# Kernel optimization log

Measured on AMD Instinct MI355X. Metric: run time of the kernel, lower is better.

The kernel has to match this reference:

```python
import jax, jax.numpy as jnp
import numpy as np

B, C, N, INPUT_DIM = 16, 19, 64, 200
VQ_DIM = 64
NUM_EMBED = 8192
FREQ = INPUT_DIM // 2 + 1  # 101 rfft bins


def setup_inputs() -> dict:
    key = jax.random.key(0)
    k_x, k_pa, k_pp, k_ca, k_cp = jax.random.split(key, 5)
    x = jax.random.normal(k_x, (B, C, N, INPUT_DIM), dtype=jnp.float32)
    # xavier_normal for [FREQ, VQ_DIM]
    std = float(np.sqrt(2.0 / (FREQ + VQ_DIM)))
    proj_amp = jax.random.normal(k_pa, (FREQ, VQ_DIM), dtype=jnp.float32) * std
    proj_phase = jax.random.normal(k_pp, (FREQ, VQ_DIM), dtype=jnp.float32) * std
    codebook_amp = jax.random.uniform(k_ca, (NUM_EMBED, VQ_DIM), dtype=jnp.float32)
    codebook_phase = jax.random.uniform(k_cp, (NUM_EMBED, VQ_DIM), dtype=jnp.float32)
    return {"x": x, "proj_amp": proj_amp, "proj_phase": proj_phase,
            "codebook_amp": codebook_amp, "codebook_phase": codebook_phase}


def _l2norm(v):
    return v / jnp.linalg.norm(v, axis=-1, keepdims=True)


def reference(x, proj_amp, proj_phase, codebook_amp, codebook_phase):
    # rfft over last dim with ortho norm -> [B,C,N,FREQ] complex
    x_fft = jnp.fft.rfft(x, axis=-1, norm="ortho")
    amp = jnp.abs(x_fft)
    phase = jnp.angle(x_fft)
    # project to vq space and L2-normalize features and codebooks
    feat_amp = _l2norm(amp @ proj_amp)        # [B,C,N,D]
    feat_phase = _l2norm(phase @ proj_phase)  # [B,C,N,D]
    cb_amp = _l2norm(codebook_amp)            # [M,D]
    cb_phase = _l2norm(codebook_phase)        # [M,D]
    # cosine similarity vs codebook, argmax over codebook axis
    sim_amp = jnp.einsum("bcnd,md->bcnm", feat_amp, cb_amp)
    sim_phase = jnp.einsum("bcnd,md->bcnm", feat_phase, cb_phase)
    idx_amp = jnp.argmax(sim_amp, axis=-1)
    idx_phase = jnp.argmax(sim_phase, axis=-1)
    return idx_amp, idx_phase
```

## Files before the change

### kernel.cpp

```cpp
#include <hip/hip_runtime.h>
#include <math.h>

constexpr int ROWS  = 19456;
constexpr int IN_DIM = 200;
constexpr int FREQ  = 101;
constexpr int VQD   = 64;
constexpr int NEMB  = 8192;
constexpr int DFT_BLOCKS = ROWS / 8;

typedef __attribute__((ext_vector_type(8))) short short8;
typedef __attribute__((ext_vector_type(4))) float floatx4;

__device__ __forceinline__ unsigned short f2bf(float v) {
    unsigned int u = __builtin_bit_cast(unsigned int, v);
    unsigned int r = u + 0x7fffu + ((u >> 16) & 1u);
    return (unsigned short)(r >> 16);
}
__device__ __forceinline__ float bf2f(unsigned short b) {
    unsigned int u = ((unsigned int)b) << 16;
    return __builtin_bit_cast(float, u);
}

__device__ __forceinline__ void cis_exact(int r, double& c, double& s) {
    if (r == 0)        { c =  1.0; s =  0.0; }
    else if (r == 50)  { c =  0.0; s = -1.0; }
    else if (r == 100) { c = -1.0; s =  0.0; }
    else if (r == 150) { c =  0.0; s =  1.0; }
    else {
        double ang = -6.283185307179586476925286766559 * (double)r / (double)IN_DIM;
        c = cos(ang); s = sin(ang);
    }
}

#define GLOAD_LDS(gp, lp) __builtin_amdgcn_global_load_lds( \
    (const __attribute__((address_space(1))) unsigned int*)(gp), \
    (__attribute__((address_space(3))) unsigned int*)(lp), 16, 0, 0)

constexpr size_t align256(size_t x) { return (x + 255) & ~(size_t)255; }
constexpr size_t SZ_FB    = (size_t)2 * ROWS * VQD * sizeof(unsigned short);
constexpr size_t OFF_FTH  = 0;
constexpr size_t OFF_FTL  = align256(OFF_FTH + SZ_FB);
constexpr size_t SZ_CBB   = (size_t)2 * NEMB * VQD * sizeof(unsigned short);
constexpr size_t OFF_CBH  = align256(OFF_FTL + SZ_FB);
constexpr size_t OFF_CBL  = align256(OFF_CBH + SZ_CBB);
constexpr size_t SZ_FD    = (size_t)2 * ROWS * VQD * sizeof(double);
constexpr size_t OFF_FD   = align256(OFF_CBL + SZ_CBB);
constexpr size_t SZ_INV   = (size_t)2 * NEMB * sizeof(double);
constexpr size_t OFF_INV  = align256(OFF_FD + SZ_FD);
constexpr size_t SZ_PI    = (size_t)2 * 4 * ROWS * sizeof(int);
constexpr size_t OFF_PI1  = align256(OFF_INV + SZ_INV);
constexpr size_t OFF_PI2  = align256(OFF_PI1 + SZ_PI);

__global__ __launch_bounds__(256) void dft_cb_kernel(
    const float* __restrict__ x, const float* __restrict__ projA, const float* __restrict__ projP,
    const float* __restrict__ cbA, const float* __restrict__ cbP,
    unsigned short* __restrict__ ftH, unsigned short* __restrict__ ftL, double* __restrict__ featD,
    unsigned short* __restrict__ cbH, unsigned short* __restrict__ cbL, double* __restrict__ invnD)
{
    __shared__ __align__(16) char smem[20064];
    const int tid = threadIdx.x;

    if (blockIdx.x >= DFT_BLOCKS) {
        float* tile = (float*)smem;
        float* inv  = (float*)(smem + 16640);
        const int bid2 = blockIdx.x - DFT_BLOCKS;
        const int which = bid2 >> 7;
        const int m0 = (bid2 & 127) * 64;
        const float* cb = which ? cbP : cbA;
        for (int e = tid; e < 4096; e += 256) {
            int c = e >> 6, d = e & 63;
            tile[c * 65 + d] = cb[(size_t)(m0 + c) * VQD + d];
        }
        __syncthreads();
        if (tid < 64) {
            double s = 0.0;
            for (int d2 = 0; d2 < 64; ++d2) { double v = (double)tile[tid * 65 + d2]; s += v * v; }
            inv[tid] = (float)(1.0 / sqrt(s));
            invnD[(size_t)which * NEMB + m0 + tid] = 1.0 / sqrt(s);
        }
        __syncthreads();
        for (int e = tid; e < 4096; e += 256) {
            int c = e >> 6, d = e & 63;
            float v = tile[c * 65 + d] * inv[c];
            unsigned short hb = f2bf(v);
            unsigned short lb = f2bf(v - bf2f(hb));
            size_t o = ((size_t)which * NEMB + m0 + c) * VQD + d;
            cbH[o] = hb; cbL[o] = lb;
        }
        return;
    }

    float*  xsT  = (float*)smem;
    float*  xpS  = (float*)(smem + 7200);
    float*  xmS  = (float*)(smem + 10400);
    float*  reS  = (float*)(smem + 13600);
    float*  imS  = (float*)(smem + 16832);
    double* cisT = (double*)(smem + 13600);
    float*  accS = (float*)(smem + 7200);
    const int r0 = blockIdx.x * 8;

    for (int e = tid; e < 8 * IN_DIM; e += 256) {
        int r = e / IN_DIM, n = e - r * IN_DIM;
        xsT[n * 9 + r] = x[(size_t)(r0 + r) * IN_DIM + n];
    }
    __syncthreads();

    for (int e = tid; e < 99 * 8; e += 256) {
        int n = (e >> 3) + 1, r = e & 7;
        float a = xsT[n * 9 + r];
        float b = xsT[(IN_DIM - n) * 9 + r];
        xpS[n * 8 + r] = a + b;
        xmS[n * 8 + r] = a - b;
    }
    if (tid < FREQ) {
        double c, s;
        cis_exact(tid, c, s);
        cisT[tid * 2]     = c;
        cisT[tid * 2 + 1] = s;
    }
    __syncthreads();

    const int k = tid & 127, half = tid >> 7;
    double c1 = 1.0, s1 = 0.0, wc = 1.0, ws = 0.0;
    if (k < FREQ) {
        c1 = cisT[k * 2]; s1 = cisT[k * 2 + 1];
        if (!half) {
            wc = c1; ws = s1;
        } else {
            switch (k & 3) {
                case 0: wc =  c1; ws =  s1; break;
                case 1: wc =  s1; ws = -c1; break;
                case 2: wc = -c1; ws = -s1; break;
                default: wc = -s1; ws =  c1; break;
            }
        }
    }
    __syncthreads();

    float re[8], im[8];
    if (k < FREQ) {
#pragma unroll
        for (int r = 0; r < 8; ++r) { re[r] = 0.f; im[r] = 0.f; }
        if (half) {
            float sg = (k & 1) ? -1.f : 1.f;
#pragma unroll
            for (int r = 0; r < 8; ++r)
                re[r] = xsT[r] + sg * xsT[100 * 9 + r];
        }
        const int n0   = half ? 51 : 1;
        const int nEnd = half ? 100 : 51;
        for (int n = n0; n < nEnd; ++n) {
            const float* xpn = xpS + n * 8;
            const float* xmn = xmS + n * 8;
            float wcf = (float)wc, wsf = (float)ws;
#pragma unroll
            for (int r = 0; r < 8; ++r) {
                re[r] = fmaf(xpn[r], wcf, re[r]);
                im[r] = fmaf(xmn[r], wsf, im[r]);
            }
            double nwc = fma(wc, c1, -ws * s1);
            double nws = fma(wc, s1,  ws * c1);
            wc = nwc; ws = nws;
        }
        if (half) {
#pragma unroll
            for (int r = 0; r < 8; ++r) { reS[k * 8 + r] = re[r]; imS[k * 8 + r] = im[r]; }
        }
    }
    __syncthreads();
    if (half == 0 && k < FREQ) {
#pragma unroll
        for (int r = 0; r < 8; ++r) {
            re[r] += reS[k * 8 + r]; im[r] += imS[k * 8 + r];
            reS[k * 8 + r] = re[r];  imS[k * 8 + r] = im[r];
        }
    }
    __syncthreads();
    for (int e = tid; e < FREQ * 8; e += 256) {
        float c = reS[e], s = imS[e];
        float a2 = fmaf(c, c, s * s);
        float ampv, phv;
        if (a2 >= 0.04f) {
            ampv = sqrtf(a2);
            phv  = atan2f(s, c);
        } else {
            const int kk = e >> 3, rr = e & 7;
            double sg = (kk & 1) ? -1.0 : 1.0;
            double reD = (double)xsT[rr] + sg * (double)xsT[100 * 9 + rr];
            double imD = 0.0;
            double cc1, ss1;
            cis_exact(kk, cc1, ss1);
            double twc = cc1, tws = ss1;
            for (int n = 1; n < 100; ++n) {
                double a = (double)xsT[n * 9 + rr];
                double b = (double)xsT[(IN_DIM - n) * 9 + rr];
                reD = fma(a + b, twc, reD);
                imD = fma(a - b, tws, imD);
                double nwc = fma(twc, cc1, -tws * ss1);
                double nws = fma(twc, ss1,  tws * cc1);
                twc = nwc; tws = nws;
            }
            ampv = (float)sqrt(reD * reD + imD * imD);
            phv  = (float)atan2(imD, reD);
        }
        reS[e] = ampv; imS[e] = phv;
    }
    __syncthreads();

    const int d = tid & 63, which = (tid >> 6) & 1, grp = tid >> 7;
    const float* proj = which ? projP : projA;
    const float* srcF = which ? imS : reS;
    float acc[8];
#pragma unroll
    for (int r = 0; r < 8; ++r) acc[r] = 0.f;
    const int kkA = grp ? 51 : 0;
    const int kkB = grp ? FREQ : 51;
    for (int kk = kkA; kk < kkB; ++kk) {
        float p = proj[kk * VQD + d];
#pragma unroll
        for (int r = 0; r < 8; ++r) acc[r] = fmaf(srcF[kk * 8 + r], p, acc[r]);
    }
    if (grp) {
#pragma unroll
        for (int r = 0; r < 8; ++r) accS[(tid & 127) * 8 + r] = acc[r];
    }
    __syncthreads();
    if (grp == 0) {
#pragma unroll
        for (int r = 0; r < 8; ++r) acc[r] += accS[tid * 8 + r];
#pragma unroll
        for (int r = 0; r < 8; ++r) {
            size_t rowi = (size_t)which * ROWS + r0 + r;
            float vf = acc[r];
            unsigned short hb = f2bf(vf);
            unsigned short lb = f2bf(vf - bf2f(hb));
            ftH[rowi * VQD + d] = hb;
            ftL[rowi * VQD + d] = lb;
            featD[rowi * VQD + d] = (double)acc[r];
        }
    }
}

#define MFMA(a, b, c) __builtin_amdgcn_mfma_f32_16x16x32_bf16(a, b, c, 0, 0, 0)
#define UPD(val, s) do { float _v = (val); \
    bool _c1 = _v > b1v[s]; bool _c2 = _v > b2v[s]; \
    b2v[s] = _c1 ? b1v[s] : (_c2 ? _v : b2v[s]); \
    b2i[s] = _c1 ? b1i[s] : (_c2 ? idx : b2i[s]); \
    b1v[s] = _c1 ? _v : b1v[s]; \
    b1i[s] = _c1 ? idx : b1i[s]; } while (0)

__global__ __launch_bounds__(256, 3) void argmax_kernel(
    const unsigned short* __restrict__ ftH, const unsigned short* __restrict__ ftL,
    const unsigned short* __restrict__ cbH, const unsigned short* __restrict__ cbL,
    int* __restrict__ pi1, int* __restrict__ pi2)
{
    __shared__ __align__(16) char lds[33792];
    const int tid = threadIdx.x;
    const int f = blockIdx.y, z = blockIdx.z;
    const int r0 = blockIdx.x * 128;
    const int w = tid >> 6, lane = tid & 63;
    const int q = lane >> 4, cl = lane & 15;

    const unsigned short* ftHb = ftH + (size_t)f * ROWS * VQD;
    const unsigned short* ftLb = ftL + (size_t)f * ROWS * VQD;
    const unsigned short* cbHb = cbH + (size_t)f * NEMB * VQD;
    const unsigned short* cbLb = cbL + (size_t)f * NEMB * VQD;

    short8 aH00, aH01, aH10, aH11, aL00, aL01, aL10, aL11;
    {
        const size_t baseA = (size_t)(r0 + w * 32 + cl) * VQD + q * 8;
        const size_t baseB = baseA + (size_t)16 * VQD;
        aH00 = *(const short8*)(ftHb + baseA);
        aH01 = *(const short8*)(ftHb + baseA + 32);
        aH10 = *(const short8*)(ftHb + baseB);
        aH11 = *(const short8*)(ftHb + baseB + 32);
        aL00 = *(const short8*)(ftLb + baseA);
        aL01 = *(const short8*)(ftLb + baseA + 32);
        aL10 = *(const short8*)(ftLb + baseB);
        aL11 = *(const short8*)(ftLb + baseB + 32);
    }

    float b1v[8], b2v[8]; int b1i[8], b2i[8];
#pragma unroll
    for (int s = 0; s < 8; ++s) { b1v[s] = -INFINITY; b2v[s] = -INFINITY; b1i[s] = 0; b2i[s] = 0; }

    const int cBase = tid >> 3;
    const int jel   = (((tid & 7) ^ (cBase & 7)) << 3);
    const unsigned short* gH = cbHb + (size_t)(z * 2048 + cBase) * VQD + jel;
    const unsigned short* gL = cbLb + (size_t)(z * 2048 + cBase) * VQD + jel;

    const int p0 = ((q ^ (cl & 7)) << 4);
    const int p1 = p0 ^ 64;

#pragma unroll
    for (int r = 0; r < 2; ++r) {
        const size_t gofs = (size_t)(32 * r) * VQD;
        GLOAD_LDS(gH + gofs, lds + w * 1024 + r * 4096);
        GLOAD_LDS(gL + gofs, lds + 8192 + w * 1024 + r * 4096);
    }

    for (int it = 0; it < 32; ++it) {
        __syncthreads();
        if (it < 31) {
            char* nbuf = lds + ((it + 1) & 1) * 16384;
            const size_t gbase = (size_t)((it + 1) * 64) * VQD;
#pragma unroll
            for (int r = 0; r < 2; ++r) {
                const size_t gofs = gbase + (size_t)(32 * r) * VQD;
                GLOAD_LDS(gH + gofs, nbuf + w * 1024 + r * 4096);
                GLOAD_LDS(gL + gofs, nbuf + 8192 + w * 1024 + r * 4096);
            }
        }

        const char* buf = lds + (it & 1) * 16384;
        const int cbase = z * 2048 + it * 64;
#pragma unroll
        for (int nt = 0; nt < 4; ++nt) {
            const char* row = buf + (nt * 16 + cl) * 128;
            short8 bH0 = *(const short8*)(row + p0);
            short8 bH1 = *(const short8*)(row + p1);
            short8 bL0 = *(const short8*)(row + 8192 + p0);
            short8 bL1 = *(const short8*)(row + 8192 + p1);

            floatx4 acc0 = {0.f, 0.f, 0.f, 0.f};
            floatx4 acc1 = {0.f, 0.f, 0.f, 0.f};
            acc0 = MFMA(aH00, bH0, acc0);  acc1 = MFMA(aH10, bH0, acc1);
            acc0 = MFMA(aH01, bH1, acc0);  acc1 = MFMA(aH11, bH1, acc1);
            acc0 = MFMA(aH00, bL0, acc0);  acc1 = MFMA(aH10, bL0, acc1);
            acc0 = MFMA(aH01, bL1, acc0);  acc1 = MFMA(aH11, bL1, acc1);
            acc0 = MFMA(aL00, bH0, acc0);  acc1 = MFMA(aL10, bH0, acc1);
            acc0 = MFMA(aL01, bH1, acc0);  acc1 = MFMA(aL11, bH1, acc1);

            const int idx = cbase + nt * 16 + cl;
#pragma unroll
            for (int i = 0; i < 4; ++i) { UPD(acc0[i], i); UPD(acc1[i], 4 + i); }
        }
    }

    __syncthreads();
    float* redv = (float*)lds;
    int*   redi = (int*)(lds + 128 * 33 * 4);
#pragma unroll
    for (int s = 0; s < 8; ++s) {
        int rowl = w * 32 + ((s & 4) << 2) + q * 4 + (s & 3);
        int base = rowl * 33 + cl * 2;
        redv[base]     = b1v[s]; redi[base]     = b1i[s];
        redv[base + 1] = b2v[s]; redi[base + 1] = b2i[s];
    }
    __syncthreads();
    if (tid < 128) {
        float v1 = -INFINITY, v2 = -INFINITY; int i1 = 0x7fffffff, i2 = 0x7fffffff;
        for (int e = 0; e < 32; ++e) {
            float v = redv[tid * 33 + e]; int id = redi[tid * 33 + e];
            if (v > v1 || (v == v1 && id < i1)) { v2 = v1; i2 = i1; v1 = v; i1 = id; }
            else if (v > v2 || (v == v2 && id < i2)) { v2 = v; i2 = id; }
        }
        size_t p = ((size_t)(f * 4 + z)) * ROWS + r0 + tid;
        pi1[p] = i1; pi2[p] = i2;
    }
}

__global__ __launch_bounds__(256) void rescore_kernel(
    const double* __restrict__ featD, const double* __restrict__ invnD,
    const float* __restrict__ cbA, const float* __restrict__ cbP,
    const int* __restrict__ pi1, const int* __restrict__ pi2,
    int* __restrict__ out)
{
    const int tid = threadIdx.x;
    const int lane = tid & 63, wave = tid >> 6;
    const int task = blockIdx.x * 4 + wave;
    const int f = task / ROWS;
    const int row = task - f * ROWS;
    const float* cb = f ? cbP : cbA;

    const int c  = lane >> 3;
    const int dp = (lane & 7) * 8;

    const int zz = c >> 1;
    const size_t p = ((size_t)(f * 4 + zz)) * ROWS + row;
    const int idx = (c & 1) ? pi2[p] : pi1[p];

    const double* fr = featD + ((size_t)f * ROWS + row) * VQD + dp;
    const float*  cr = cb + (size_t)idx * VQD + dp;
    double t = 0.0;
#pragma unroll
    for (int j = 0; j < 8; ++j) t = fma(fr[j], (double)cr[j], t);
    t += __shfl_xor(t, 1, 64);
    t += __shfl_xor(t, 2, 64);
    t += __shfl_xor(t, 4, 64);
    double bv = t * invnD[(size_t)f * NEMB + idx];
    int    bi = idx;
#pragma unroll
    for (int m = 8; m <= 32; m <<= 1) {
        double ov = __shfl_xor(bv, m, 64);
        int    oi = __shfl_xor(bi, m, 64);
        if (ov > bv || (ov == bv && oi < bi)) { bv = ov; bi = oi; }
    }
    if (lane == 0) out[task] = bi;
}

extern "C" void kernel_launch(void* const* d_in, const int* in_sizes, int n_in,
                              void* d_out, int out_size, void* d_ws, size_t ws_size,
                              hipStream_t stream)
{
    const float* x     = (const float*)d_in[0];
    const float* projA = (const float*)d_in[1];
    const float* projP = (const float*)d_in[2];
    const float* cbA   = (const float*)d_in[3];
    const float* cbP   = (const float*)d_in[4];

    char* ws = (char*)d_ws;
    unsigned short* ftH   = (unsigned short*)(ws + OFF_FTH);
    unsigned short* ftL   = (unsigned short*)(ws + OFF_FTL);
    unsigned short* cbHp  = (unsigned short*)(ws + OFF_CBH);
    unsigned short* cbLp  = (unsigned short*)(ws + OFF_CBL);
    double*         featD = (double*)(ws + OFF_FD);
    double*         invnD = (double*)(ws + OFF_INV);
    int*            pi1   = (int*)(ws + OFF_PI1);
    int*            pi2   = (int*)(ws + OFF_PI2);

    dft_cb_kernel<<<DFT_BLOCKS + 256, 256, 0, stream>>>(
        x, projA, projP, cbA, cbP, ftH, ftL, featD, cbHp, cbLp, invnD);
    argmax_kernel<<<dim3(ROWS / 128, 2, 4), 256, 0, stream>>>(ftH, ftL, cbHp, cbLp, pi1, pi2);
    rescore_kernel<<<(2 * ROWS) / 4, 256, 0, stream>>>(featD, invnD, cbA, cbP, pi1, pi2, (int*)d_out);
}
```

Measured before the change: 276.1 us.

## Precompute DFT twiddle table once and compute the DFT with two waves per block

Adds a single-block prep kernel that writes a float twiddle table (cos/sin per frequency and sample) to workspace, replacing the per-thread double-precision twiddle recurrence inside the DFT loop. The DFT phase now runs on only two waves, each lane covering two frequencies and reading twiddles from global/L2. This removes FP64 FMAs from the inner loop but idles half the block's waves and adds a small serial kernel launch plus global twiddle loads per iteration.

```diff
diff --git a/kernel.cpp b/kernel.cpp
--- a/kernel.cpp
+++ b/kernel.cpp
@@ -50,10 +50,44 @@
 constexpr size_t SZ_PI    = (size_t)2 * 4 * ROWS * sizeof(int);
 constexpr size_t OFF_PI1  = align256(OFF_INV + SZ_INV);
 constexpr size_t OFF_PI2  = align256(OFF_PI1 + SZ_PI);
+constexpr size_t SZ_TW    = (size_t)100 * 128 * 2 * sizeof(float);
+constexpr size_t OFF_TW   = align256(OFF_PI2 + SZ_PI);
+
+__global__ __launch_bounds__(128) void twiddle_prep(float* __restrict__ twT)
+{
+    const int k = threadIdx.x;
+    if (k >= FREQ) {
+        for (int n = 1; n < 100; ++n) { twT[(n * 128 + k) * 2] = 0.f; twT[(n * 128 + k) * 2 + 1] = 0.f; }
+        return;
+    }
+    double c1, s1;
+    cis_exact(k, c1, s1);
+    double wc = c1, ws = s1;
+    for (int n = 1; n < 51; ++n) {
+        twT[(n * 128 + k) * 2]     = (float)wc;
+        twT[(n * 128 + k) * 2 + 1] = (float)ws;
+        double nwc = fma(wc, c1, -ws * s1);
+        double nws = fma(wc, s1,  ws * c1);
+        wc = nwc; ws = nws;
+    }
+    switch (k & 3) {
+        case 0: wc =  c1; ws =  s1; break;
+        case 1: wc =  s1; ws = -c1; break;
+        case 2: wc = -c1; ws = -s1; break;
+        default: wc = -s1; ws =  c1; break;
+    }
+    for (int n = 51; n < 100; ++n) {
+        twT[(n * 128 + k) * 2]     = (float)wc;
+        twT[(n * 128 + k) * 2 + 1] = (float)ws;
+        double nwc = fma(wc, c1, -ws * s1);
+        double nws = fma(wc, s1,  ws * c1);
+        wc = nwc; ws = nws;
+    }
+}
 
 __global__ __launch_bounds__(256) void dft_cb_kernel(
     const float* __restrict__ x, const float* __restrict__ projA, const float* __restrict__ projP,
-    const float* __restrict__ cbA, const float* __restrict__ cbP,
+    const float* __restrict__ cbA, const float* __restrict__ cbP, const float* __restrict__ twT,
     unsigned short* __restrict__ ftH, unsigned short* __restrict__ ftL, double* __restrict__ featD,
     unsigned short* __restrict__ cbH, unsigned short* __restrict__ cbL, double* __restrict__ invnD)
 {
@@ -95,7 +129,6 @@
     float*  xmS  = (float*)(smem + 10400);
     float*  reS  = (float*)(smem + 13600);
     float*  imS  = (float*)(smem + 16832);
-    double* cisT = (double*)(smem + 13600);
     float*  accS = (float*)(smem + 7200);
     const int r0 = blockIdx.x * 8;
 
@@ -112,67 +145,63 @@
         xpS[n * 8 + r] = a + b;
         xmS[n * 8 + r] = a - b;
     }
-    if (tid < FREQ) {
-        double c, s;
-        cis_exact(tid, c, s);
-        cisT[tid * 2]     = c;
-        cisT[tid * 2 + 1] = s;
-    }
-    __syncthreads();
-
-    const int k = tid & 127, half = tid >> 7;
-    double c1 = 1.0, s1 = 0.0, wc = 1.0, ws = 0.0;
-    if (k < FREQ) {
-        c1 = cisT[k * 2]; s1 = cisT[k * 2 + 1];
-        if (!half) {
-            wc = c1; ws = s1;
-        } else {
-            switch (k & 3) {
-                case 0: wc =  c1; ws =  s1; break;
-                case 1: wc =  s1; ws = -c1; break;
-                case 2: wc = -c1; ws = -s1; break;
-                default: wc = -s1; ws =  c1; break;
-            }
-        }
-    }
-    __syncthreads();
-
-    float re[8], im[8];
-    if (k < FREQ) {
-#pragma unroll
-        for (int r = 0; r < 8; ++r) { re[r] = 0.f; im[r] = 0.f; }
+    __syncthreads();
+
+    const int lane = tid & 63, wv = tid >> 6;
+    const int k1 = lane, k2 = lane + 64;
+    float re1[8], im1[8], re2[8], im2[8];
+    if (wv < 2) {
+        const int half = wv;
+#pragma unroll
+        for (int r = 0; r < 8; ++r) { re1[r] = 0.f; im1[r] = 0.f; re2[r] = 0.f; im2[r] = 0.f; }
         if (half) {
-            float sg = (k & 1) ? -1.f : 1.f;
-#pragma unroll
-            for (int r = 0; r < 8; ++r)
-                re[r] = xsT[r] + sg * xsT[100 * 9 + r];
+            float sg1 = (k1 & 1) ? -1.f : 1.f;
+            float sg2 = (k2 & 1) ? -1.f : 1.f;
+#pragma unroll
+            for (int r = 0; r < 8; ++r) {
+                float a0 = xsT[r], a100 = xsT[100 * 9 + r];
+                re1[r] = a0 + sg1 * a100;
+                re2[r] = a0 + sg2 * a100;
+            }
         }
         const int n0   = half ? 51 : 1;
         const int nEnd = half ? 100 : 51;
         for (int n = n0; n < nEnd; ++n) {
             const float* xpn = xpS + n * 8;
             const float* xmn = xmS + n * 8;
-            float wcf = (float)wc, wsf = (float)ws;
+            const float2 t1 = *(const float2*)(twT + (size_t)(n * 128 + k1) * 2);
+            const float2 t2 = *(const float2*)(twT + (size_t)(n * 128 + k2) * 2);
 #pragma unroll
             for (int r = 0; r < 8; ++r) {
-                re[r] = fmaf(xpn[r], wcf, re[r]);
-                im[r] = fmaf(xmn[r], wsf, im[r]);
-            }
-            double nwc = fma(wc, c1, -ws * s1);
-            double nws = fma(wc, s1,  ws * c1);
-            wc = nwc; ws = nws;
+                float xpr = xpn[r], xmr = xmn[r];
+                re1[r] = fmaf(xpr, t1.x, re1[r]);
+                im1[r] = fmaf(xmr, t1.y, im1[r]);
+                re2[r] = fmaf(xpr, t2.x, re2[r]);
+                im2[r] = fmaf(xmr, t2.y, im2[r]);
+            }
         }
         if (half) {
 #pragma unroll
-            for (int r = 0; r < 8; ++r) { reS[k * 8 + r] = re[r]; imS[k * 8 + r] = im[r]; }
-        }
-    }
-    __syncthreads();
-    if (half == 0 && k < FREQ) {
+            for (int r = 0; r < 8; ++r) { reS[k1 * 8 + r] = re1[r]; imS[k1 * 8 + r] = im1[r]; }
+            if (k2 < FREQ) {
+#pragma unroll
+                for (int r = 0; r < 8; ++r) { reS[k2 * 8 + r] = re2[r]; imS[k2 * 8 + r] = im2[r]; }
+            }
+        }
+    }
+    __syncthreads();
+    if (wv == 0) {
 #pragma unroll
         for (int r = 0; r < 8; ++r) {
-            re[r] += reS[k * 8 + r]; im[r] += imS[k * 8 + r];
-            reS[k * 8 + r] = re[r];  imS[k * 8 + r] = im[r];
+            re1[r] += reS[k1 * 8 + r]; im1[r] += imS[k1 * 8 + r];
+            reS[k1 * 8 + r] = re1[r];  imS[k1 * 8 + r] = im1[r];
+        }
+        if (k2 < FREQ) {
+#pragma unroll
+            for (int r = 0; r < 8; ++r) {
+                re2[r] += reS[k2 * 8 + r]; im2[r] += imS[k2 * 8 + r];
+                reS[k2 * 8 + r] = re2[r];  imS[k2 * 8 + r] = im2[r];
+            }
         }
     }
     __syncthreads();
@@ -418,9 +447,11 @@
     double*         invnD = (double*)(ws + OFF_INV);
     int*            pi1   = (int*)(ws + OFF_PI1);
     int*            pi2   = (int*)(ws + OFF_PI2);
-
+    float*          twT   = (float*)(ws + OFF_TW);
+
+    twiddle_prep<<<1, 128, 0, stream>>>(twT);
     dft_cb_kernel<<<DFT_BLOCKS + 256, 256, 0, stream>>>(
-        x, projA, projP, cbA, cbP, ftH, ftL, featD, cbHp, cbLp, invnD);
+        x, projA, projP, cbA, cbP, twT, ftH, ftL, featD, cbHp, cbLp, invnD);
     argmax_kernel<<<dim3(ROWS / 128, 2, 4), 256, 0, stream>>>(ftH, ftL, cbHp, cbLp, pi1, pi2);
     rescore_kernel<<<(2 * ROWS) / 4, 256, 0, stream>>>(featD, invnD, cbA, cbP, pi1, pi2, (int*)d_out);
 }
```

Result: slower. 293.4 us (+6.2%).

## Use radix-4 decimation to split DFT by frequency parity

Applied to the files above, without the earlier changes.

Replaces the symmetric real-DFT (x[n]±x[N-n]) with a radix-4 style split of the 200-point input into four 50-sample quarters. Even frequencies read precombined sums selected by k mod 4, and odd frequencies use complex differences twiddled by the 8th roots of unity. Each thread now covers 25 samples instead of about 50, and wavefronts are divided by frequency parity and sample half. This is meant to cut the per-block DFT inner-loop work, at the cost of more complex indexing and possibly different rounding.

```diff
diff --git a/kernel.cpp b/kernel.cpp
--- a/kernel.cpp
+++ b/kernel.cpp
@@ -91,8 +91,10 @@
     }
 
     float*  xsT  = (float*)smem;
-    float*  xpS  = (float*)(smem + 7200);
-    float*  xmS  = (float*)(smem + 10400);
+    float*  e0S  = (float*)(smem + 7200);
+    float*  e2S  = (float*)(smem + 8800);
+    float*  d02S = (float*)(smem + 10400);
+    float*  d13S = (float*)(smem + 12000);
     float*  reS  = (float*)(smem + 13600);
     float*  imS  = (float*)(smem + 16832);
     double* cisT = (double*)(smem + 13600);
@@ -105,12 +107,18 @@
     }
     __syncthreads();
 
-    for (int e = tid; e < 99 * 8; e += 256) {
-        int n = (e >> 3) + 1, r = e & 7;
-        float a = xsT[n * 9 + r];
-        float b = xsT[(IN_DIM - n) * 9 + r];
-        xpS[n * 8 + r] = a + b;
-        xmS[n * 8 + r] = a - b;
+    for (int e = tid; e < 50 * 8; e += 256) {
+        int b = e >> 3, r = e & 7;
+        float x0 = xsT[b * 9 + r];
+        float x1 = xsT[(50 + b) * 9 + r];
+        float x2 = xsT[(100 + b) * 9 + r];
+        float x3 = xsT[(150 + b) * 9 + r];
+        float s02 = x0 + x2, dd02 = x0 - x2;
+        float s13 = x1 + x3, dd13 = x3 - x1;
+        e0S[e]  = s02 + s13;
+        e2S[e]  = s02 - s13;
+        d02S[e] = dd02;
+        d13S[e] = dd13;
     }
     if (tid < FREQ) {
         double c, s;
@@ -120,55 +128,77 @@
     }
     __syncthreads();
 
-    const int k = tid & 127, half = tid >> 7;
+    const int lane = tid & 63, wv = tid >> 6;
+    const int parity = wv & 1, bgrp = wv >> 1;
+    const int k = 2 * lane + parity;
+    const bool act = (k < FREQ);
+
     double c1 = 1.0, s1 = 0.0, wc = 1.0, ws = 0.0;
-    if (k < FREQ) {
+    if (act) {
         c1 = cisT[k * 2]; s1 = cisT[k * 2 + 1];
-        if (!half) {
-            wc = c1; ws = s1;
+        if (bgrp) {
+            const double RH = 0.70710678118654752440;
+            switch (k & 7) {
+                case 0:  wc =  1.0; ws =  0.0; break;
+                case 1:  wc =  RH;  ws = -RH;  break;
+                case 2:  wc =  0.0; ws = -1.0; break;
+                case 3:  wc = -RH;  ws = -RH;  break;
+                case 4:  wc = -1.0; ws =  0.0; break;
+                case 5:  wc = -RH;  ws =  RH;  break;
+                case 6:  wc =  0.0; ws =  1.0; break;
+                default: wc =  RH;  ws =  RH;  break;
+            }
+        }
+    }
+    __syncthreads();
+
+    float re[8], im[8];
+    if (act) {
+#pragma unroll
+        for (int r = 0; r < 8; ++r) { re[r] = 0.f; im[r] = 0.f; }
+        const int b0 = bgrp * 25;
+        if (parity == 0) {
+            const float* Y = (k & 2) ? e2S : e0S;
+            for (int j = 0; j < 25; ++j) {
+                const float* Yb = Y + (b0 + j) * 8;
+                float wcf = (float)wc, wsf = (float)ws;
+#pragma unroll
+                for (int r = 0; r < 8; ++r) {
+                    float y = Yb[r];
+                    re[r] = fmaf(y, wcf, re[r]);
+                    im[r] = fmaf(y, wsf, im[r]);
+                }
+                double nwc = fma(wc, c1, -ws * s1);
+                double nws = fma(wc, s1,  ws * c1);
+                wc = nwc; ws = nws;
+            }
         } else {
-            switch (k & 3) {
-                case 0: wc =  c1; ws =  s1; break;
-                case 1: wc =  s1; ws = -c1; break;
-                case 2: wc = -c1; ws = -s1; break;
-                default: wc = -s1; ws =  c1; break;
+            const float tq = (k & 2) ? -1.f : 1.f;
+            for (int j = 0; j < 25; ++j) {
+                const float* Ar = d02S + (b0 + j) * 8;
+                const float* Ai = d13S + (b0 + j) * 8;
+                float wcf = (float)wc, wsf = (float)ws;
+                float u = tq * wcf, v = tq * wsf;
+#pragma unroll
+                for (int r = 0; r < 8; ++r) {
+                    float ar = Ar[r], ai = Ai[r];
+                    re[r] = fmaf(ar, wcf, re[r]);
+                    re[r] = fmaf(ai, -v,  re[r]);
+                    im[r] = fmaf(ar, wsf, im[r]);
+                    im[r] = fmaf(ai, u,   im[r]);
+                }
+                double nwc = fma(wc, c1, -ws * s1);
+                double nws = fma(wc, s1,  ws * c1);
+                wc = nwc; ws = nws;
             }
         }
-    }
-    __syncthreads();
-
-    float re[8], im[8];
-    if (k < FREQ) {
-#pragma unroll
-        for (int r = 0; r < 8; ++r) { re[r] = 0.f; im[r] = 0.f; }
-        if (half) {
-            float sg = (k & 1) ? -1.f : 1.f;
-#pragma unroll
-            for (int r = 0; r < 8; ++r)
-                re[r] = xsT[r] + sg * xsT[100 * 9 + r];
-        }
-        const int n0   = half ? 51 : 1;
-        const int nEnd = half ? 100 : 51;
-        for (int n = n0; n < nEnd; ++n) {
-            const float* xpn = xpS + n * 8;
-            const float* xmn = xmS + n * 8;
-            float wcf = (float)wc, wsf = (float)ws;
-#pragma unroll
-            for (int r = 0; r < 8; ++r) {
-                re[r] = fmaf(xpn[r], wcf, re[r]);
-                im[r] = fmaf(xmn[r], wsf, im[r]);
-            }
-            double nwc = fma(wc, c1, -ws * s1);
-            double nws = fma(wc, s1,  ws * c1);
-            wc = nwc; ws = nws;
-        }
-        if (half) {
+        if (bgrp == 1) {
 #pragma unroll
             for (int r = 0; r < 8; ++r) { reS[k * 8 + r] = re[r]; imS[k * 8 + r] = im[r]; }
         }
     }
     __syncthreads();
-    if (half == 0 && k < FREQ) {
+    if (bgrp == 0 && act) {
 #pragma unroll
         for (int r = 0; r < 8; ++r) {
             re[r] += reS[k * 8 + r]; im[r] += imS[k * 8 + r];
```

After: 271.1 us. No clear change (-1.8%).
